# Optimization experiments

Measured on AMD Instinct MI355X. Metric: run time of the kernel, lower is better.

The kernel has to match this reference:

```python
import jax, jax.numpy as jnp
import numpy as np

N = 30000      # nodes
E = 480000     # edges (before self-loops)
F_IN = 128     # dim_in
H = 8          # heads
C = 32         # dim_h (per-head channels)
F_H = H * C    # concat hidden width = 256
NEG_SLOPE = 0.2


def setup_inputs() -> dict:
    key = jax.random.key(0)
    ks = jax.random.split(key, 12)
    def glorot(k, shape, fan):
        return jax.random.normal(k, shape, jnp.float32) * (1.0 / np.sqrt(fan))
    return {
        "x": jax.random.normal(ks[0], (N, F_IN), jnp.float32),
        "edge_index": jax.random.randint(ks[1], (2, E), 0, N),
        "W1": glorot(ks[2], (F_IN, F_H), F_IN),
        "a1_src": glorot(ks[3], (H, C), C),
        "a1_dst": glorot(ks[4], (H, C), C),
        "b1": jnp.zeros((F_H,), jnp.float32),
        "W2": glorot(ks[5], (F_H, F_H), F_H),
        "a2_src": glorot(ks[6], (H, C), C),
        "a2_dst": glorot(ks[7], (H, C), C),
        "b2": jnp.zeros((F_H,), jnp.float32),
        "Wl": glorot(ks[8], (F_H, 1), F_H),
        "bl": jnp.zeros((1,), jnp.float32),
    }


def gat_conv(x, src, dst, W, a_src, a_dst, b):
    """PyG-style GATConv (concat=True, add_self_loops handled by caller)."""
    n = x.shape[0]
    h = (x @ W).reshape(n, H, C)                       # [N,H,C]
    alpha_s = jnp.einsum('nhc,hc->nh', h, a_src)        # [N,H]
    alpha_d = jnp.einsum('nhc,hc->nh', h, a_dst)        # [N,H]
    e = jax.nn.leaky_relu(alpha_s[src] + alpha_d[dst], NEG_SLOPE)  # [E,H]
    # segment softmax over incoming edges of each destination node
    e_max = jax.ops.segment_max(e, dst, num_segments=n)            # [N,H]
    e_max = jnp.where(jnp.isfinite(e_max), e_max, 0.0)
    e_exp = jnp.exp(e - e_max[dst])                                # [E,H]
    denom = jax.ops.segment_sum(e_exp, dst, num_segments=n)        # [N,H]
    alpha = e_exp / (denom[dst] + 1e-16)                           # [E,H]
    out = jax.ops.segment_sum(h[src] * alpha[:, :, None], dst, num_segments=n)  # [N,H,C]
    return out.reshape(n, F_H) + b


def reference(x, edge_index, W1, a1_src, a1_dst, b1, W2, a2_src, a2_dst, b2, Wl, bl):
    loops = jnp.arange(N, dtype=edge_index.dtype)      # self-loops (PyG default)
    src = jnp.concatenate([edge_index[0], loops])
    dst = jnp.concatenate([edge_index[1], loops])
    h = jax.nn.elu(gat_conv(x, src, dst, W1, a1_src, a1_dst, b1))
    h = jax.nn.elu(gat_conv(h, src, dst, W2, a2_src, a2_dst, b2))
    return (h @ Wl + bl).squeeze(1)                    # [N]
```

## Files before the change

### kernel.cpp

```cpp
#include <hip/hip_runtime.h>
#include <hip/hip_bf16.h>

#define NNODES 30000
#define NEDGES 480000
#define TE (NEDGES + NNODES)
#define FH 256
#define NH 8
#define NSB ((NNODES + 255) / 256)

typedef unsigned short ushort_t;
typedef __attribute__((ext_vector_type(8))) _Float16 f16x8;
typedef __attribute__((ext_vector_type(2))) _Float16 f16x2;
typedef __attribute__((ext_vector_type(4))) float f32x4;

__global__ void zero_counts(int* __restrict__ c) {
    int i = blockIdx.x * 256 + threadIdx.x;
    if (i < NNODES) c[i] = 0;
}

__global__ void count_kernel(const int* __restrict__ ei, int* __restrict__ counts) {
    int e = blockIdx.x * 256 + threadIdx.x;
    if (e >= TE) return;
    int d = (e < NEDGES) ? ei[NEDGES + e] : (e - NEDGES);
    atomicAdd(&counts[d], 1);
}

__global__ __launch_bounds__(256) void scan1_kernel(const int* __restrict__ counts,
                                                    int* __restrict__ rp,
                                                    int* __restrict__ bsum) {
    __shared__ int s[256];
    const int tid = threadIdx.x;
    const int i = blockIdx.x * 256 + tid;
    int v = (i < NNODES) ? counts[i] : 0;
    s[tid] = v;
    __syncthreads();
    for (int off = 1; off < 256; off <<= 1) {
        int t = (tid >= off) ? s[tid - off] : 0;
        __syncthreads();
        s[tid] += t;
        __syncthreads();
    }
    if (i < NNODES) rp[i] = s[tid] - v;
    if (tid == 255) bsum[blockIdx.x] = s[255];
}

__global__ __launch_bounds__(128) void scan2_kernel(int* __restrict__ bsum) {
    __shared__ int s[128];
    const int tid = threadIdx.x;
    int v = (tid < NSB) ? bsum[tid] : 0;
    s[tid] = v;
    __syncthreads();
    for (int off = 1; off < 128; off <<= 1) {
        int t = (tid >= off) ? s[tid - off] : 0;
        __syncthreads();
        s[tid] += t;
        __syncthreads();
    }
    if (tid < NSB) bsum[tid] = s[tid] - v;
}

__global__ __launch_bounds__(256) void scan3_kernel(int* __restrict__ rp,
                                                    const int* __restrict__ bsum,
                                                    int* __restrict__ cursor) {
    const int i = blockIdx.x * 256 + threadIdx.x;
    if (i < NNODES) {
        int r = rp[i] + bsum[blockIdx.x];
        rp[i] = r;
        cursor[i] = r;
    }
    if (i == 0) rp[NNODES] = TE;
}

__global__ void fill_kernel(const int* __restrict__ ei, int* __restrict__ cursor,
                            int* __restrict__ ssrc) {
    int e = blockIdx.x * 256 + threadIdx.x;
    if (e >= TE) return;
    int s, d;
    if (e < NEDGES) { s = ei[e]; d = ei[NEDGES + e]; }
    else            { s = e - NEDGES; d = s; }
    int pos = atomicAdd(&cursor[d], 1);
    ssrc[pos] = s;
}

__device__ __forceinline__ unsigned f2h2(float a, float b) {
    f16x2 h;
    h.x = (_Float16)a;
    h.y = (_Float16)b;
    return __builtin_bit_cast(unsigned, h);
}

__global__ void cvt_x_kernel(const float* __restrict__ X,
                             _Float16* __restrict__ out, int nquads) {
    int i = blockIdx.x * 256 + threadIdx.x;
    if (i >= nquads) return;
    float4 v = *reinterpret_cast<const float4*>(&X[(size_t)i * 4]);
    uint2 st;
    st.x = f2h2(v.x, v.y);
    st.y = f2h2(v.z, v.w);
    *reinterpret_cast<uint2*>(&out[(size_t)i * 4]) = st;
}

template<int K>
__global__ void cvtT_w(const float* __restrict__ W, _Float16* __restrict__ t) {
    int idx = blockIdx.x * 256 + threadIdx.x;
    if (idx >= 256 * K) return;
    int n = idx & 255, k = idx >> 8;
    t[n * K + k] = (_Float16)W[idx];
}

template<int K>
__global__ __launch_bounds__(256) void gemm_mfma(
    const _Float16* __restrict__ A,  const _Float16* __restrict__ Bt,
    const float* __restrict__ ASRC, const float* __restrict__ ADST,
    _Float16* __restrict__ HFh, float* __restrict__ AS, float* __restrict__ AD) {

    constexpr int LDK = 40;
    __shared__ _Float16 Ah[128][LDK], Bh[128][LDK];

    const int tid  = threadIdx.x;
    const int lane = tid & 63;
    const int wid  = tid >> 6;
    const int m0 = blockIdx.x * 128;
    const int n0 = blockIdx.y * 128;
    const int wm = (wid & 1) * 64, wn = (wid >> 1) * 64;
    const int q = lane >> 4;
    const int c = lane & 15;

    f32x4 acc[4][4];
#pragma unroll
    for (int mi = 0; mi < 4; ++mi)
#pragma unroll
        for (int ni = 0; ni < 4; ++ni) acc[mi][ni] = (f32x4){0.f, 0.f, 0.f, 0.f};

    for (int k0 = 0; k0 < K; k0 += 32) {
        __syncthreads();
#pragma unroll
        for (int rep = 0; rep < 2; ++rep) {
            int idx = tid + 256 * rep;
            int row = idx >> 2;
            int ch  = (idx & 3) * 8;
            int gr = m0 + row;
            uint4 v = make_uint4(0u, 0u, 0u, 0u);
            if (gr < NNODES)
                v = *reinterpret_cast<const uint4*>(&A[(size_t)gr * K + k0 + ch]);
            *reinterpret_cast<uint4*>(&Ah[row][ch]) = v;
            uint4 bv = *reinterpret_cast<const uint4*>(&Bt[(size_t)(n0 + row) * K + k0 + ch]);
            *reinterpret_cast<uint4*>(&Bh[row][ch]) = bv;
        }
        __syncthreads();

        const int koff = q * 8;
        f16x8 fa[4], fb[4];
#pragma unroll
        for (int mi = 0; mi < 4; ++mi)
            fa[mi] = *reinterpret_cast<const f16x8*>(&Ah[wm + mi * 16 + c][koff]);
#pragma unroll
        for (int ni = 0; ni < 4; ++ni)
            fb[ni] = *reinterpret_cast<const f16x8*>(&Bh[wn + ni * 16 + c][koff]);
#pragma unroll
        for (int mi = 0; mi < 4; ++mi)
#pragma unroll
            for (int ni = 0; ni < 4; ++ni)
                acc[mi][ni] = __builtin_amdgcn_mfma_f32_16x16x32_f16(fa[mi], fb[ni], acc[mi][ni], 0, 0, 0);
    }

    float as_v[4], ad_v[4];
#pragma unroll
    for (int ni = 0; ni < 4; ++ni) {
        as_v[ni] = ASRC[n0 + wn + ni * 16 + c];
        ad_v[ni] = ADST[n0 + wn + ni * 16 + c];
    }
    const int head0 = (n0 + wn) >> 5;

#pragma unroll
    for (int mi = 0; mi < 4; ++mi) {
#pragma unroll
        for (int j = 0; j < 4; ++j) {
            int row = m0 + wm + mi * 16 + q * 4 + j;
            bool ok = row < NNODES;
            if (ok) {
#pragma unroll
                for (int ni = 0; ni < 4; ++ni)
                    HFh[(size_t)row * FH + n0 + wn + ni * 16 + c] = (_Float16)acc[mi][ni][j];
            }
            float ps0 = acc[mi][0][j] * as_v[0] + acc[mi][1][j] * as_v[1];
            float ps1 = acc[mi][2][j] * as_v[2] + acc[mi][3][j] * as_v[3];
            float pd0 = acc[mi][0][j] * ad_v[0] + acc[mi][1][j] * ad_v[1];
            float pd1 = acc[mi][2][j] * ad_v[2] + acc[mi][3][j] * ad_v[3];
#pragma unroll
            for (int off = 8; off >= 1; off >>= 1) {
                ps0 += __shfl_xor(ps0, off);
                ps1 += __shfl_xor(ps1, off);
                pd0 += __shfl_xor(pd0, off);
                pd1 += __shfl_xor(pd1, off);
            }
            if (ok && c == 0) {
                AS[row * NH + head0]     = ps0;
                AS[row * NH + head0 + 1] = ps1;
                AD[row * NH + head0]     = pd0;
                AD[row * NH + head0 + 1] = pd1;
            }
        }
    }
}

template<bool FINAL>
__global__ __launch_bounds__(256) void aggregate(
    const _Float16* __restrict__ HFh,
    const float* __restrict__ AS, const float* __restrict__ AD,
    const int* __restrict__ rp, const int* __restrict__ ssrc,
    const float* __restrict__ BIAS,
    _Float16* __restrict__ X2H,
    const float* __restrict__ WL, const float* __restrict__ BL,
    float* __restrict__ OUT) {

    __shared__ float wslab[4][64 * 9];

    const int tid  = threadIdx.x;
    const int lane = tid & 63;
    const int wid  = tid >> 6;
    const int node = __builtin_amdgcn_readfirstlane(blockIdx.x * 4 + wid);
    const int epar = lane >> 5;
    const int cg   = lane & 31;
    const int hh   = cg >> 2;
    const int c8   = cg * 8;
    float* wl = wslab[wid];

    const int p0  = rp[node];
    const int deg = rp[node + 1] - p0;

    const float4 ad0 = *reinterpret_cast<const float4*>(&AD[node * NH]);
    const float4 ad1 = *reinterpret_cast<const float4*>(&AD[node * NH + 4]);

    float a0=0.f,a1=0.f,a2=0.f,a3=0.f,a4=0.f,a5=0.f,a6=0.f,a7=0.f;
    float den = 0.f;

    for (int base = 0; base < deg; base += 64) {
        const int ne = min(64, deg - base);

        if (lane < ne) {
            int s = ssrc[p0 + base + lane];
            float4 as0 = *reinterpret_cast<const float4*>(&AS[s * NH]);
            float4 as1 = *reinterpret_cast<const float4*>(&AS[s * NH + 4]);
            float sv[8] = {as0.x + ad0.x, as0.y + ad0.y, as0.z + ad0.z, as0.w + ad0.w,
                           as1.x + ad1.x, as1.y + ad1.y, as1.z + ad1.z, as1.w + ad1.w};
            float* wp = &wl[lane * 9];
#pragma unroll
            for (int h = 0; h < 8; ++h) {
                float t = sv[h] > 0.f ? sv[h] : 0.2f * sv[h];
                wp[h] = __expf(t);
            }
        }
        asm volatile("s_waitcnt lgkmcnt(0)" ::: "memory");

        for (int e0 = 0; e0 < ne; e0 += 2) {
            const int  e   = e0 + epar;
            const bool act = e < ne;
            const int  ee  = act ? e : 0;
            const int  sa  = ssrc[p0 + base + ee];
            const float wr = wl[ee * 9 + hh];
            const float w  = act ? wr : 0.f;
            den += w;
            const f16x8 hv = *reinterpret_cast<const f16x8*>(&HFh[(size_t)sa * FH + c8]);
            a0 = fmaf((float)hv[0], w, a0);
            a1 = fmaf((float)hv[1], w, a1);
            a2 = fmaf((float)hv[2], w, a2);
            a3 = fmaf((float)hv[3], w, a3);
            a4 = fmaf((float)hv[4], w, a4);
            a5 = fmaf((float)hv[5], w, a5);
            a6 = fmaf((float)hv[6], w, a6);
            a7 = fmaf((float)hv[7], w, a7);
        }
    }

    a0 += __shfl_xor(a0, 32); a1 += __shfl_xor(a1, 32);
    a2 += __shfl_xor(a2, 32); a3 += __shfl_xor(a3, 32);
    a4 += __shfl_xor(a4, 32); a5 += __shfl_xor(a5, 32);
    a6 += __shfl_xor(a6, 32); a7 += __shfl_xor(a7, 32);
    den += __shfl_xor(den, 32);

    const float inv = 1.f / (den + 1e-16f);
    const float4 b0 = *reinterpret_cast<const float4*>(&BIAS[c8]);
    const float4 b1 = *reinterpret_cast<const float4*>(&BIAS[c8 + 4]);
    float o[8];
    o[0] = fmaf(a0, inv, b0.x); o[1] = fmaf(a1, inv, b0.y);
    o[2] = fmaf(a2, inv, b0.z); o[3] = fmaf(a3, inv, b0.w);
    o[4] = fmaf(a4, inv, b1.x); o[5] = fmaf(a5, inv, b1.y);
    o[6] = fmaf(a6, inv, b1.z); o[7] = fmaf(a7, inv, b1.w);
#pragma unroll
    for (int j = 0; j < 8; ++j) o[j] = o[j] > 0.f ? o[j] : expm1f(o[j]);

    if (!FINAL) {
        uint2 st;
        st.x = f2h2(o[epar * 4 + 0], o[epar * 4 + 1]);
        st.y = f2h2(o[epar * 4 + 2], o[epar * 4 + 3]);
        *reinterpret_cast<uint2*>(&X2H[(size_t)node * FH + c8 + epar * 4]) = st;
    } else {
        const float4 w0 = *reinterpret_cast<const float4*>(&WL[c8]);
        const float4 w1 = *reinterpret_cast<const float4*>(&WL[c8 + 4]);
        float pl = fmaf(o[0], w0.x, fmaf(o[1], w0.y, fmaf(o[2], w0.z, o[3] * w0.w)));
        pl = fmaf(o[4], w1.x, fmaf(o[5], w1.y, fmaf(o[6], w1.z, fmaf(o[7], w1.w, pl))));
#pragma unroll
        for (int off = 16; off >= 1; off >>= 1) pl += __shfl_xor(pl, off);
        if (lane == 0) OUT[node] = pl + BL[0];
    }
}

extern "C" void kernel_launch(void* const* d_in, const int* in_sizes, int n_in,
                              void* d_out, int out_size, void* d_ws, size_t ws_size,
                              hipStream_t stream) {
    const float* x   = (const float*)d_in[0];
    const int*   ei  = (const int*)d_in[1];
    const float* W1  = (const float*)d_in[2];
    const float* a1s = (const float*)d_in[3];
    const float* a1d = (const float*)d_in[4];
    const float* b1  = (const float*)d_in[5];
    const float* W2  = (const float*)d_in[6];
    const float* a2s = (const float*)d_in[7];
    const float* a2d = (const float*)d_in[8];
    const float* b2  = (const float*)d_in[9];
    const float* Wl  = (const float*)d_in[10];
    const float* bl  = (const float*)d_in[11];
    float* out = (float*)d_out;

    char* w = (char*)d_ws;
    auto alloc = [&](size_t bytes) -> char* {
        char* p = w;
        w += (bytes + 255) & ~size_t(255);
        return p;
    };
    int*   counts = (int*)alloc((size_t)NNODES * 4);
    int*   rp     = (int*)alloc((size_t)(NNODES + 1) * 4);
    int*   cursor = (int*)alloc((size_t)NNODES * 4);
    int*   bsum   = (int*)alloc((size_t)NSB * 4);
    int*   ssrc   = (int*)alloc((size_t)TE * 4);
    _Float16* hfh = (_Float16*)alloc((size_t)NNODES * FH * 2);
    _Float16* x1h = (_Float16*)alloc((size_t)NNODES * 128 * 2);
    _Float16* x2h = (_Float16*)alloc((size_t)NNODES * FH * 2);
    float* asb    = (float*)alloc((size_t)NNODES * NH * 4);
    float* adb    = (float*)alloc((size_t)NNODES * NH * 4);
    _Float16* w1t = (_Float16*)alloc((size_t)128 * 256 * 2);
    _Float16* w2t = (_Float16*)alloc((size_t)256 * 256 * 2);

    zero_counts<<<NSB, 256, 0, stream>>>(counts);
    count_kernel<<<(TE + 255) / 256, 256, 0, stream>>>(ei, counts);
    scan1_kernel<<<NSB, 256, 0, stream>>>(counts, rp, bsum);
    scan2_kernel<<<1, 128, 0, stream>>>(bsum);
    scan3_kernel<<<NSB, 256, 0, stream>>>(rp, bsum, cursor);
    fill_kernel<<<(TE + 255) / 256, 256, 0, stream>>>(ei, cursor, ssrc);

    const int xq = NNODES * 128 / 4;
    cvt_x_kernel<<<(xq + 255) / 256, 256, 0, stream>>>(x, x1h, xq);
    cvtT_w<128><<<128, 256, 0, stream>>>(W1, w1t);
    cvtT_w<256><<<256, 256, 0, stream>>>(W2, w2t);

    const dim3 ggrid((NNODES + 127) / 128, 2);
    gemm_mfma<128><<<ggrid, 256, 0, stream>>>(x1h, w1t, a1s, a1d, hfh, asb, adb);
    aggregate<false><<<NNODES / 4, 256, 0, stream>>>(hfh, asb, adb, rp, ssrc, b1,
                                                     x2h, nullptr, nullptr, nullptr);
    gemm_mfma<256><<<ggrid, 256, 0, stream>>>(x2h, w2t, a2s, a2d, hfh, asb, adb);
    aggregate<true><<<NNODES / 4, 256, 0, stream>>>(hfh, asb, adb, rp, ssrc, b2,
                                                    nullptr, Wl, bl, out);
}
```

Before: 199.7 us.

## Fuse x fp16 conversion into GEMM and cache edge sources in LDS

Removes the standalone fp32-to-fp16 conversion kernel for x by converting on the fly while loading A tiles in the first GEMM. In aggregation, the per-edge source index is stashed in the LDS weight slab (stride raised to 10) so the inner loop reads it from LDS instead of re-reading ssrc from global memory. The inner edge loop is also unrolled by 4. The GEMM reads more bytes of fp32 for layer 1 since both column blocks convert the same rows, and the LDS stride change may alter bank conflicts.

```diff
diff --git a/kernel.cpp b/kernel.cpp
--- a/kernel.cpp
+++ b/kernel.cpp
@@ -89,17 +89,6 @@
     return __builtin_bit_cast(unsigned, h);
 }
 
-__global__ void cvt_x_kernel(const float* __restrict__ X,
-                             _Float16* __restrict__ out, int nquads) {
-    int i = blockIdx.x * 256 + threadIdx.x;
-    if (i >= nquads) return;
-    float4 v = *reinterpret_cast<const float4*>(&X[(size_t)i * 4]);
-    uint2 st;
-    st.x = f2h2(v.x, v.y);
-    st.y = f2h2(v.z, v.w);
-    *reinterpret_cast<uint2*>(&out[(size_t)i * 4]) = st;
-}
-
 template<int K>
 __global__ void cvtT_w(const float* __restrict__ W, _Float16* __restrict__ t) {
     int idx = blockIdx.x * 256 + threadIdx.x;
@@ -108,9 +97,9 @@
     t[n * K + k] = (_Float16)W[idx];
 }
 
-template<int K>
+template<int K, bool CVT>
 __global__ __launch_bounds__(256) void gemm_mfma(
-    const _Float16* __restrict__ A,  const _Float16* __restrict__ Bt,
+    const void* __restrict__ Araw,  const _Float16* __restrict__ Bt,
     const float* __restrict__ ASRC, const float* __restrict__ ADST,
     _Float16* __restrict__ HFh, float* __restrict__ AS, float* __restrict__ AD) {
 
@@ -141,8 +130,18 @@
             int ch  = (idx & 3) * 8;
             int gr = m0 + row;
             uint4 v = make_uint4(0u, 0u, 0u, 0u);
-            if (gr < NNODES)
-                v = *reinterpret_cast<const uint4*>(&A[(size_t)gr * K + k0 + ch]);
+            if (gr < NNODES) {
+                if (CVT) {
+                    const float* Xf = (const float*)Araw;
+                    float4 f0 = *reinterpret_cast<const float4*>(&Xf[(size_t)gr * K + k0 + ch]);
+                    float4 f1 = *reinterpret_cast<const float4*>(&Xf[(size_t)gr * K + k0 + ch + 4]);
+                    v.x = f2h2(f0.x, f0.y); v.y = f2h2(f0.z, f0.w);
+                    v.z = f2h2(f1.x, f1.y); v.w = f2h2(f1.z, f1.w);
+                } else {
+                    const _Float16* Ah_g = (const _Float16*)Araw;
+                    v = *reinterpret_cast<const uint4*>(&Ah_g[(size_t)gr * K + k0 + ch]);
+                }
+            }
             *reinterpret_cast<uint4*>(&Ah[row][ch]) = v;
             uint4 bv = *reinterpret_cast<const uint4*>(&Bt[(size_t)(n0 + row) * K + k0 + ch]);
             *reinterpret_cast<uint4*>(&Bh[row][ch]) = bv;
@@ -214,7 +213,7 @@
     const float* __restrict__ WL, const float* __restrict__ BL,
     float* __restrict__ OUT) {
 
-    __shared__ float wslab[4][64 * 9];
+    __shared__ float wslab[4][64 * 10];
 
     const int tid  = threadIdx.x;
     const int lane = tid & 63;
@@ -244,21 +243,23 @@
             float4 as1 = *reinterpret_cast<const float4*>(&AS[s * NH + 4]);
             float sv[8] = {as0.x + ad0.x, as0.y + ad0.y, as0.z + ad0.z, as0.w + ad0.w,
                            as1.x + ad1.x, as1.y + ad1.y, as1.z + ad1.z, as1.w + ad1.w};
-            float* wp = &wl[lane * 9];
+            float* wp = &wl[lane * 10];
 #pragma unroll
             for (int h = 0; h < 8; ++h) {
                 float t = sv[h] > 0.f ? sv[h] : 0.2f * sv[h];
                 wp[h] = __expf(t);
             }
+            wp[8] = __int_as_float(s);
         }
         asm volatile("s_waitcnt lgkmcnt(0)" ::: "memory");
 
+#pragma unroll 4
         for (int e0 = 0; e0 < ne; e0 += 2) {
             const int  e   = e0 + epar;
             const bool act = e < ne;
             const int  ee  = act ? e : 0;
-            const int  sa  = ssrc[p0 + base + ee];
-            const float wr = wl[ee * 9 + hh];
+            const int  sa  = __float_as_int(wl[ee * 10 + 8]);
+            const float wr = wl[ee * 10 + hh];
             const float w  = act ? wr : 0.f;
             den += w;
             const f16x8 hv = *reinterpret_cast<const f16x8*>(&HFh[(size_t)sa * FH + c8]);
@@ -335,7 +336,6 @@
     int*   bsum   = (int*)alloc((size_t)NSB * 4);
     int*   ssrc   = (int*)alloc((size_t)TE * 4);
     _Float16* hfh = (_Float16*)alloc((size_t)NNODES * FH * 2);
-    _Float16* x1h = (_Float16*)alloc((size_t)NNODES * 128 * 2);
     _Float16* x2h = (_Float16*)alloc((size_t)NNODES * FH * 2);
     float* asb    = (float*)alloc((size_t)NNODES * NH * 4);
     float* adb    = (float*)alloc((size_t)NNODES * NH * 4);
@@ -349,16 +349,14 @@
     scan3_kernel<<<NSB, 256, 0, stream>>>(rp, bsum, cursor);
     fill_kernel<<<(TE + 255) / 256, 256, 0, stream>>>(ei, cursor, ssrc);
 
-    const int xq = NNODES * 128 / 4;
-    cvt_x_kernel<<<(xq + 255) / 256, 256, 0, stream>>>(x, x1h, xq);
     cvtT_w<128><<<128, 256, 0, stream>>>(W1, w1t);
     cvtT_w<256><<<256, 256, 0, stream>>>(W2, w2t);
 
     const dim3 ggrid((NNODES + 127) / 128, 2);
-    gemm_mfma<128><<<ggrid, 256, 0, stream>>>(x1h, w1t, a1s, a1d, hfh, asb, adb);
+    gemm_mfma<128, true><<<ggrid, 256, 0, stream>>>(x, w1t, a1s, a1d, hfh, asb, adb);
     aggregate<false><<<NNODES / 4, 256, 0, stream>>>(hfh, asb, adb, rp, ssrc, b1,
                                                      x2h, nullptr, nullptr, nullptr);
-    gemm_mfma<256><<<ggrid, 256, 0, stream>>>(x2h, w2t, a2s, a2d, hfh, asb, adb);
+    gemm_mfma<256, false><<<ggrid, 256, 0, stream>>>(x2h, w2t, a2s, a2d, hfh, asb, adb);
     aggregate<true><<<NNODES / 4, 256, 0, stream>>>(hfh, asb, adb, rp, ssrc, b2,
                                                     nullptr, Wl, bl, out);
 }
```

Result: faster. 180.4 us (-9.7%).
